# Kernel tuning notes

Hardware: AMD Instinct MI355X
Metric: run time of the kernel (lower is better)

Reference implementation:

```python
import jax, jax.numpy as jnp
import numpy as np

N = 100000
E = 800000
D_IN = 64
D_OUT = 64
SCALES = (4, 8)


def setup_inputs() -> dict:
    key = jax.random.key(0)
    ks = jax.random.split(key, 8)
    x = jax.random.normal(ks[0], (N, D_IN), dtype=jnp.float32)
    edge_index = jax.random.randint(ks[1], (2, E), 0, N, dtype=jnp.int64)
    s = 1.0 / np.sqrt(D_IN)
    W1 = jax.random.uniform(ks[2], (D_OUT, D_IN), minval=-s, maxval=s, dtype=jnp.float32)
    b1 = jax.random.uniform(ks[3], (D_OUT,), minval=-s, maxval=s, dtype=jnp.float32)
    W2 = jax.random.uniform(ks[4], (D_OUT, D_IN), minval=-s, maxval=s, dtype=jnp.float32)
    b2 = jax.random.uniform(ks[5], (D_OUT,), minval=-s, maxval=s, dtype=jnp.float32)
    sg = 1.0 / np.sqrt(D_OUT * len(SCALES))
    Wg = jax.random.uniform(ks[6], (D_OUT, D_OUT * len(SCALES)), minval=-sg, maxval=sg, dtype=jnp.float32)
    bg = jax.random.uniform(ks[7], (D_OUT,), minval=-sg, maxval=sg, dtype=jnp.float32)
    return {"x": x, "edge_index": edge_index, "W1": W1, "b1": b1,
            "W2": W2, "b2": b2, "Wg": Wg, "bg": bg}


def _gconv(x, src, tgt, W, b):
    # scatter-add neighbor features: agg[src] += x[tgt]
    agg = jax.ops.segment_sum(x[tgt], src, num_segments=N)  # [N, D_IN]
    counts = jax.ops.segment_sum(jnp.ones((src.shape[0], 1), x.dtype), src,
                                 num_segments=N) + 1e-6     # [N, 1]
    agg = agg / counts
    return agg @ W.T + b                                    # [N, D_OUT]


def reference(x, edge_index, W1, b1, W2, b2, Wg, bg):
    k_max = E // N  # = 8
    outs = []
    for scale, (W, b) in zip(SCALES, ((W1, b1), (W2, b2))):
        scale = min(scale, k_max)
        src = edge_index[0, :N * scale]
        tgt = edge_index[1, :N * scale]
        outs.append(_gconv(x, src, tgt, W, b))
    multi = jnp.concatenate(outs, axis=-1)                   # [N, 2*D_OUT]
    gate = jax.nn.sigmoid(multi @ Wg.T + bg)                 # [N, D_OUT]
    fused = gate * outs[0] + (1.0 - gate) * outs[1]
    return fused
```

## Files before the change

### kernel.cpp

```cpp
#include <hip/hip_runtime.h>
#include <hip/hip_bf16.h>

#define N_NODES 100000
#define E_TOTAL 800000
#define E1      400000
#define D       64
#define CAP     32

#define NPB        256
#define NB         ((N_NODES + NPB - 1) / NPB)
#define BSTRIDE    (NPB * CAP)
#define BCAP       3072
#define EPB        4096
#define NBKT_BLKS  ((E_TOTAL + EPB - 1) / EPB)

typedef short s16x8 __attribute__((ext_vector_type(8)));
typedef float f32x4 __attribute__((ext_vector_type(4)));
typedef unsigned u32x4 __attribute__((ext_vector_type(4)));

#define WS_CNT     0
#define WS_ENTRIES (N_NODES)
#define WS_W1B     (WS_ENTRIES + N_NODES * CAP)
#define WS_W2B     (WS_W1B + 2048)
#define WS_WGB     (WS_W2B + 2048)
#define WS_BIAS    (WS_WGB + 4096)
#define WS_CUR     (WS_BIAS + 192)
#define WS_XB      (WS_CUR + 400)
#define WS_NEED_BYTES ((size_t)(WS_XB + (size_t)N_NODES * D / 2) * 4)

#define R_X   (N_NODES * D / 8)
#define R_W   (R_X + 2048)
#define R_B   (R_W + 24)
#define CONV_BLOCKS ((R_B + 255) / 256)

__device__ __forceinline__ float ldv(const void* p, size_t idx, int fp32)
{
    return fp32 ? ((const float*)p)[idx]
                : __bfloat162float(((const __hip_bfloat16*)p)[idx]);
}

__device__ __forceinline__ void detect2(const int* ei, const unsigned short* xu,
                                        int* s2, int& e64, int& fp32)
{
    if (threadIdx.x == 0) { s2[0] = 0; s2[1] = 0; }
    __syncthreads();
    if (threadIdx.x < 16 && ei[2 * threadIdx.x + 1] != 0) atomicOr(&s2[0], 1);
    { unsigned u = xu[threadIdx.x]; if (((u >> 7) & 0xFF) >= 0x90) atomicOr(&s2[1], 1); }
    __syncthreads();
    e64 = (s2[0] == 0); fp32 = s2[1];
}

__global__ __launch_bounds__(256) void prep_kernel(
    const void* __restrict__ xv, const int* __restrict__ ei,
    const void* __restrict__ W1v, const void* __restrict__ b1v,
    const void* __restrict__ W2v, const void* __restrict__ b2v,
    const void* __restrict__ Wgv, const void* __restrict__ bgv,
    unsigned* __restrict__ ws, int use_xb)
{
    __shared__ int s2[2];
    __shared__ unsigned hist[NB];
    __shared__ unsigned bbase[NB];
    int e64, fp32;
    detect2(ei, (const unsigned short*)xv, s2, e64, fp32);

    if (blockIdx.x < NBKT_BLKS) {
        for (int j = threadIdx.x; j < NB; j += 256) hist[j] = 0;
        __syncthreads();

        const int e0 = blockIdx.x * EPB;
        int srcv[16], tgtv[16];
#pragma unroll
        for (int i = 0; i < 16; ++i) {
            const int e = e0 + i * 256 + threadIdx.x;
            srcv[i] = -1;
            if (e < E_TOTAL) {
                if (e64) {
                    srcv[i] = (int)((const uint2*)ei)[e].x;
                    tgtv[i] = (int)((const uint2*)ei)[E_TOTAL + e].x;
                } else {
                    srcv[i] = ei[e]; tgtv[i] = ei[E_TOTAL + e];
                }
            }
        }
        unsigned recv[16], br[16];
#pragma unroll
        for (int i = 0; i < 16; ++i) {
            const int e = e0 + i * 256 + threadIdx.x;
            br[i] = 0xFFFFFFFFu;
            if (srcv[i] >= 0) {
                const unsigned b = (unsigned)srcv[i] >> 8;
                const unsigned r = atomicAdd(&hist[b], 1u);
                recv[i] = (unsigned)tgtv[i]
                        | ((e < E1) ? (1u << 17) : 0u)
                        | (((unsigned)srcv[i] & (NPB - 1)) << 18);
                br[i] = (b << 16) | r;
            }
        }
        __syncthreads();
        for (int j = threadIdx.x; j < NB; j += 256) {
            const unsigned h = hist[j];
            bbase[j] = h ? atomicAdd(ws + WS_CUR + j, h) : 0u;
        }
        __syncthreads();
#pragma unroll
        for (int i = 0; i < 16; ++i) {
            if (br[i] != 0xFFFFFFFFu) {
                const unsigned b = br[i] >> 16, r = br[i] & 0xFFFFu;
                const unsigned pos = bbase[b] + r;
                if (pos < BCAP)
                    ws[WS_ENTRIES + (size_t)b * BSTRIDE + pos] = recv[i];
            }
        }
        return;
    }

    const int gid = (blockIdx.x - NBKT_BLKS) * 256 + threadIdx.x;
    __hip_bfloat16* Xb  = (__hip_bfloat16*)(ws + WS_XB);
    __hip_bfloat16* W1b = (__hip_bfloat16*)(ws + WS_W1B);
    __hip_bfloat16* W2b = (__hip_bfloat16*)(ws + WS_W2B);
    __hip_bfloat16* Wgb = (__hip_bfloat16*)(ws + WS_WGB);
    float* bias = (float*)(ws + WS_BIAS);

    if (gid < R_X) {
        if (use_xb && fp32) {
            const f32x4 v0 = ((const f32x4*)xv)[2 * gid];
            const f32x4 v1 = ((const f32x4*)xv)[2 * gid + 1];
            s16x8 o;
#pragma unroll
            for (int j = 0; j < 4; ++j) {
                o[j]     = (short)__bfloat16_as_ushort(__float2bfloat16(v0[j]));
                o[4 + j] = (short)__bfloat16_as_ushort(__float2bfloat16(v1[j]));
            }
            *(s16x8*)(Xb + (size_t)gid * 8) = o;
        }
    } else if (gid < R_W) {
        const int j = gid - R_X;
#pragma unroll
        for (int k = 0; k < 8; ++k) {
            const int i = j * 8 + k;
            if (i < 4096)       W1b[i]        = __float2bfloat16(ldv(W1v, i, fp32));
            else if (i < 8192)  W2b[i - 4096] = __float2bfloat16(ldv(W2v, i - 4096, fp32));
            else                Wgb[i - 8192] = __float2bfloat16(ldv(Wgv, i - 8192, fp32));
        }
    } else if (gid < R_B) {
        const int j = gid - R_W;
#pragma unroll
        for (int k = 0; k < 8; ++k) {
            const int i = j * 8 + k;
            if (i < 64)       bias[i] = ldv(b1v, i, fp32);
            else if (i < 128) bias[i] = ldv(b2v, i - 64, fp32);
            else              bias[i] = ldv(bgv, i - 128, fp32);
        }
    }
}

__global__ __launch_bounds__(256) void csr_kernel(unsigned* __restrict__ ws)
{
    __shared__ unsigned cnt_l[NPB];
    __shared__ __align__(16) unsigned ent[NPB * CAP];

    const int b  = blockIdx.x;
    const int n0 = b * NPB;
    const int nn = min(NPB, N_NODES - n0);

    cnt_l[threadIdx.x] = 0;
    __syncthreads();

    const unsigned C = min(ws[WS_CUR + b], (unsigned)BCAP);
    for (unsigned r = threadIdx.x; r < C; r += 256) {
        const unsigned rec = ws[WS_ENTRIES + (size_t)b * BSTRIDE + r];
        const unsigned sl  = rec >> 18;
        const unsigned p   = atomicAdd(&cnt_l[sl], 1u);
        if (p < CAP)
            ent[sl * CAP + p] = (rec & 0x1FFFFu) | ((rec & (1u << 17)) ? 0x80000000u : 0u);
    }
    __syncthreads();

    const int tot4 = (nn * CAP) / 4;
    u32x4* dst = (u32x4*)(ws + WS_ENTRIES + (size_t)n0 * CAP);
    const u32x4* srcp = (const u32x4*)ent;
    for (int j = threadIdx.x; j < tot4; j += 256) dst[j] = srcp[j];

    if (threadIdx.x < nn) ws[WS_CNT + n0 + threadIdx.x] = cnt_l[threadIdx.x];
}

__global__ __launch_bounds__(256) void fused_kernel(
    const unsigned* __restrict__ ws, const void* __restrict__ xv,
    void* __restrict__ outv, int use_xb)
{
    __shared__ __align__(16) __hip_bfloat16 sS[16][136];
    __shared__ __align__(16) __hip_bfloat16 sO[16][136];
    __shared__ int s2d[2];

    if (threadIdx.x == 0) s2d[0] = 0;
    __syncthreads();
    { unsigned u = ((const unsigned short*)xv)[threadIdx.x];
      if (((u >> 7) & 0xFF) >= 0x90) atomicOr(&s2d[0], 1); }
    __syncthreads();
    const int fp32 = s2d[0];

    const int w    = threadIdx.x >> 6;
    const int lane = threadIdx.x & 63;
    const int base = blockIdx.x * 16;

    const int direct_f32 = (fp32 && !use_xb);
    const char* xb = (use_xb && fp32) ? (const char*)(ws + WS_XB) : (const char*)xv;
    const float* xf = (const float*)xv;

    unsigned eraw[4], entv[4], degr[4]; int degc[4];
#pragma unroll
    for (int i = 0; i < 4; ++i) {
        const int n = base + w * 4 + i;
        degr[i] = ws[WS_CNT + n];
        eraw[i] = (lane < CAP) ? ws[WS_ENTRIES + (size_t)n * CAP + lane] : 0u;
    }
#pragma unroll
    for (int i = 0; i < 4; ++i) {
        degc[i] = (int)min(degr[i], (unsigned)CAP);
        entv[i] = (lane < degc[i]) ? eraw[i] : 0u;
    }

    const int half = lane >> 5;
    const int cc   = lane & 31;

    if (!direct_f32) {
        int c1[4];
#pragma unroll
        for (int i = 0; i < 4; ++i)
            c1[i] = (int)__popcll(__ballot(entv[i] & 0x80000000u));

        float s1x[4], s1y[4], s2x[4], s2y[4];
#pragma unroll
        for (int i = 0; i < 4; ++i) { s1x[i] = s1y[i] = s2x[i] = s2y[i] = 0.f; }

        int rmax = 0;
#pragma unroll
        for (int i = 0; i < 4; ++i) rmax = max(rmax, (degc[i] + 1) >> 1);

#pragma unroll 2
        for (int r = 0; r < rmax; ++r) {
#pragma unroll
            for (int i = 0; i < 4; ++i) {
                const int j = 2 * r + half;
                const unsigned en = __shfl(entv[i], j);
                if (j < degc[i]) {
                    const unsigned off = ((en & 0x7FFFFFFFu) << 7) + ((unsigned)cc << 2);
                    const unsigned u = *(const unsigned*)(xb + off);
                    const float fx = __uint_as_float(u << 16);
                    const float fy = __uint_as_float(u & 0xFFFF0000u);
                    const float fl = (en & 0x80000000u) ? 1.f : 0.f;
                    s2x[i] += fx; s2y[i] += fy;
                    s1x[i] = fmaf(fl, fx, s1x[i]); s1y[i] = fmaf(fl, fy, s1y[i]);
                }
            }
        }

#pragma unroll
        for (int i = 0; i < 4; ++i) {
            const int nl = w * 4 + i;
            float a = s1x[i], b = s1y[i], c = s2x[i], d = s2y[i];
            a += __shfl_xor(a, 32); b += __shfl_xor(b, 32);
            c += __shfl_xor(c, 32); d += __shfl_xor(d, 32);
            const float inv1 = 1.0f / ((float)c1[i] + 1e-6f);
            const float inv2 = 1.0f / ((float)degr[i] + 1e-6f);
            if (lane < 32) {
                const __hip_bfloat162 p1 = __float22bfloat162_rn({a * inv1, b * inv1});
                const __hip_bfloat162 p2 = __float22bfloat162_rn({c * inv2, d * inv2});
                *(__hip_bfloat162*)&sS[nl][2 * cc]      = p1;
                *(__hip_bfloat162*)&sS[nl][64 + 2 * cc] = p2;
            }
        }
    } else {
#pragma unroll
        for (int i = 0; i < 4; ++i) {
            const int nl = w * 4 + i;
            const int c1 = (int)__popcll(__ballot(entv[i] & 0x80000000u));
            float s1x = 0.f, s2x = 0.f;
            for (int j = 0; j < degc[i]; ++j) {
                const unsigned en = __builtin_amdgcn_readlane(entv[i], j);
                const float v = xf[(size_t)(en & 0x7FFFFFFFu) * D + lane];
                s2x += v;
                if (en & 0x80000000u) s1x += v;
            }
            const float inv1 = 1.0f / ((float)c1 + 1e-6f);
            const float inv2 = 1.0f / ((float)degr[i] + 1e-6f);
            sS[nl][lane]      = __float2bfloat16(s1x * inv1);
            sS[nl][64 + lane] = __float2bfloat16(s2x * inv2);
        }
    }
    __syncthreads();

    const int m = lane & 15;
    const int q = lane >> 4;
    const int nd = w * 16 + m;

    const s16x8* W1b = (const s16x8*)(ws + WS_W1B);
    const s16x8* W2b = (const s16x8*)(ws + WS_W2B);
    const s16x8* Wgb = (const s16x8*)(ws + WS_WGB);
    const float* bias = (const float*)(ws + WS_BIAS);

    const s16x8 a1c0 = *(const s16x8*)&sS[m][q * 8];
    const s16x8 a1c1 = *(const s16x8*)&sS[m][32 + q * 8];
    const s16x8 a2c0 = *(const s16x8*)&sS[m][64 + q * 8];
    const s16x8 a2c1 = *(const s16x8*)&sS[m][96 + q * 8];

    f32x4 z = {0.f, 0.f, 0.f, 0.f};
    z = __builtin_amdgcn_mfma_f32_16x16x32_bf16(a1c0, W1b[nd * 8 + q],     z, 0, 0, 0);
    z = __builtin_amdgcn_mfma_f32_16x16x32_bf16(a1c1, W1b[nd * 8 + 4 + q], z, 0, 0, 0);
    f32x4 y = {0.f, 0.f, 0.f, 0.f};
    y = __builtin_amdgcn_mfma_f32_16x16x32_bf16(a2c0, W2b[nd * 8 + q],     y, 0, 0, 0);
    y = __builtin_amdgcn_mfma_f32_16x16x32_bf16(a2c1, W2b[nd * 8 + 4 + q], y, 0, 0, 0);
    const float bb1 = bias[nd], bb2 = bias[64 + nd];
#pragma unroll
    for (int r = 0; r < 4; ++r) { z[r] += bb1; y[r] += bb2; }

#pragma unroll
    for (int r = 0; r < 4; ++r) {
        sO[q * 4 + r][nd]      = __float2bfloat16(z[r]);
        sO[q * 4 + r][64 + nd] = __float2bfloat16(y[r]);
    }
    __syncthreads();

    s16x8 ga[4];
#pragma unroll
    for (int c = 0; c < 4; ++c)
        ga[c] = *(const s16x8*)&sO[m][c * 32 + q * 8];

    f32x4 g4 = {0.f, 0.f, 0.f, 0.f};
#pragma unroll
    for (int c = 0; c < 4; ++c)
        g4 = __builtin_amdgcn_mfma_f32_16x16x32_bf16(ga[c], Wgb[nd * 16 + c * 4 + q], g4, 0, 0, 0);
    const float bbg = bias[128 + nd];

#pragma unroll
    for (int r = 0; r < 4; ++r) {
        const float g = 1.0f / (1.0f + __expf(-(g4[r] + bbg)));
        const float v = g * z[r] + (1.0f - g) * y[r];
        const size_t node = (size_t)(base + q * 4 + r);
        if (fp32) ((float*)outv)[node * 64 + nd] = v;
        else      ((__hip_bfloat16*)outv)[node * 64 + nd] = __float2bfloat16(v);
    }
}

extern "C" void kernel_launch(void* const* d_in, const int* in_sizes, int n_in,
                              void* d_out, int out_size, void* d_ws, size_t ws_size,
                              hipStream_t stream)
{
    const void* x  = d_in[0];
    const int*  ei = (const int*)d_in[1];
    unsigned* ws = (unsigned*)d_ws;

    const int use_xb = (ws_size >= WS_NEED_BYTES) ? 1 : 0;

    hipMemsetAsync(ws + WS_CUR, 0, NB * sizeof(unsigned), stream);
    prep_kernel<<<NBKT_BLKS + CONV_BLOCKS, 256, 0, stream>>>(
        x, ei, d_in[2], d_in[3], d_in[4], d_in[5], d_in[6], d_in[7], ws, use_xb);
    csr_kernel<<<NB, 256, 0, stream>>>(ws);
    fused_kernel<<<N_NODES / 16, 256, 0, stream>>>(ws, x, d_out, use_xb);
}
```

Before: 171.6 us.

## Halve CSR bucket size, move x-to-bf16 conversion into CSR kernel, unroll gather

Bucket width drops from 256 to 128 nodes, which doubles the number of CSR blocks and halves the per-block shared-memory footprint. The fp32-to-bf16 conversion of x moves out of the edge-bucketing kernel and into the CSR kernel as extra blocks, to balance work across the two launches. The gather loop becomes branch-free: masked lanes load from row 0 and are zeroed, the trip count is rounded up to a multiple of four, and unrolling goes from 2 to 4 to expose more loads in flight. The cost is extra wasted loads in the padded iterations, and a per-bucket capacity of 1536 that could overflow if the edge distribution is skewed.

Result: faster. 150.8 us (-12.1%).

```diff
diff --git a/kernel.cpp b/kernel.cpp
--- a/kernel.cpp
+++ b/kernel.cpp
@@ -7,10 +7,10 @@
 #define D       64
 #define CAP     32
 
-#define NPB        256
+#define NPB        128
 #define NB         ((N_NODES + NPB - 1) / NPB)
 #define BSTRIDE    (NPB * CAP)
-#define BCAP       3072
+#define BCAP       1536
 #define EPB        4096
 #define NBKT_BLKS  ((E_TOTAL + EPB - 1) / EPB)
 
@@ -25,13 +25,14 @@
 #define WS_WGB     (WS_W2B + 2048)
 #define WS_BIAS    (WS_WGB + 4096)
 #define WS_CUR     (WS_BIAS + 192)
-#define WS_XB      (WS_CUR + 400)
+#define WS_XB      (WS_CUR + 800)
 #define WS_NEED_BYTES ((size_t)(WS_XB + (size_t)N_NODES * D / 2) * 4)
 
-#define R_X   (N_NODES * D / 8)
-#define R_W   (R_X + 2048)
-#define R_B   (R_W + 24)
-#define CONV_BLOCKS ((R_B + 255) / 256)
+#define PREP_CONV_THREADS (2048 + 24)
+#define PREP_CONV_BLOCKS  ((PREP_CONV_THREADS + 255) / 256)
+
+#define R_X          (N_NODES * D / 8)
+#define XCONV_BLOCKS (R_X / 256)
 
 __device__ __forceinline__ float ldv(const void* p, size_t idx, int fp32)
 {
@@ -55,7 +56,7 @@
     const void* __restrict__ W1v, const void* __restrict__ b1v,
     const void* __restrict__ W2v, const void* __restrict__ b2v,
     const void* __restrict__ Wgv, const void* __restrict__ bgv,
-    unsigned* __restrict__ ws, int use_xb)
+    unsigned* __restrict__ ws)
 {
     __shared__ int s2[2];
     __shared__ unsigned hist[NB];
@@ -88,7 +89,7 @@
             const int e = e0 + i * 256 + threadIdx.x;
             br[i] = 0xFFFFFFFFu;
             if (srcv[i] >= 0) {
-                const unsigned b = (unsigned)srcv[i] >> 8;
+                const unsigned b = (unsigned)srcv[i] >> 7;
                 const unsigned r = atomicAdd(&hist[b], 1u);
                 recv[i] = (unsigned)tgtv[i]
                         | ((e < E1) ? (1u << 17) : 0u)
@@ -115,35 +116,21 @@
     }
 
     const int gid = (blockIdx.x - NBKT_BLKS) * 256 + threadIdx.x;
-    __hip_bfloat16* Xb  = (__hip_bfloat16*)(ws + WS_XB);
     __hip_bfloat16* W1b = (__hip_bfloat16*)(ws + WS_W1B);
     __hip_bfloat16* W2b = (__hip_bfloat16*)(ws + WS_W2B);
     __hip_bfloat16* Wgb = (__hip_bfloat16*)(ws + WS_WGB);
     float* bias = (float*)(ws + WS_BIAS);
 
-    if (gid < R_X) {
-        if (use_xb && fp32) {
-            const f32x4 v0 = ((const f32x4*)xv)[2 * gid];
-            const f32x4 v1 = ((const f32x4*)xv)[2 * gid + 1];
-            s16x8 o;
-#pragma unroll
-            for (int j = 0; j < 4; ++j) {
-                o[j]     = (short)__bfloat16_as_ushort(__float2bfloat16(v0[j]));
-                o[4 + j] = (short)__bfloat16_as_ushort(__float2bfloat16(v1[j]));
-            }
-            *(s16x8*)(Xb + (size_t)gid * 8) = o;
-        }
-    } else if (gid < R_W) {
-        const int j = gid - R_X;
+    if (gid < 2048) {
 #pragma unroll
         for (int k = 0; k < 8; ++k) {
-            const int i = j * 8 + k;
+            const int i = gid * 8 + k;
             if (i < 4096)       W1b[i]        = __float2bfloat16(ldv(W1v, i, fp32));
             else if (i < 8192)  W2b[i - 4096] = __float2bfloat16(ldv(W2v, i - 4096, fp32));
             else                Wgb[i - 8192] = __float2bfloat16(ldv(Wgv, i - 8192, fp32));
         }
-    } else if (gid < R_B) {
-        const int j = gid - R_W;
+    } else if (gid < 2072) {
+        const int j = gid - 2048;
 #pragma unroll
         for (int k = 0; k < 8; ++k) {
             const int i = j * 8 + k;
@@ -154,34 +141,60 @@
     }
 }
 
-__global__ __launch_bounds__(256) void csr_kernel(unsigned* __restrict__ ws)
+__global__ __launch_bounds__(256) void csr_kernel(
+    const void* __restrict__ xv, unsigned* __restrict__ ws, int use_xb)
 {
     __shared__ unsigned cnt_l[NPB];
     __shared__ __align__(16) unsigned ent[NPB * CAP];
-
-    const int b  = blockIdx.x;
-    const int n0 = b * NPB;
-    const int nn = min(NPB, N_NODES - n0);
-
-    cnt_l[threadIdx.x] = 0;
-    __syncthreads();
-
-    const unsigned C = min(ws[WS_CUR + b], (unsigned)BCAP);
-    for (unsigned r = threadIdx.x; r < C; r += 256) {
-        const unsigned rec = ws[WS_ENTRIES + (size_t)b * BSTRIDE + r];
-        const unsigned sl  = rec >> 18;
-        const unsigned p   = atomicAdd(&cnt_l[sl], 1u);
-        if (p < CAP)
-            ent[sl * CAP + p] = (rec & 0x1FFFFu) | ((rec & (1u << 17)) ? 0x80000000u : 0u);
-    }
-    __syncthreads();
-
-    const int tot4 = (nn * CAP) / 4;
-    u32x4* dst = (u32x4*)(ws + WS_ENTRIES + (size_t)n0 * CAP);
-    const u32x4* srcp = (const u32x4*)ent;
-    for (int j = threadIdx.x; j < tot4; j += 256) dst[j] = srcp[j];
-
-    if (threadIdx.x < nn) ws[WS_CNT + n0 + threadIdx.x] = cnt_l[threadIdx.x];
+    __shared__ int s2[1];
+
+    if (blockIdx.x < NB) {
+        const int b  = blockIdx.x;
+        const int n0 = b * NPB;
+        const int nn = min(NPB, N_NODES - n0);
+
+        if (threadIdx.x < NPB) cnt_l[threadIdx.x] = 0;
+        __syncthreads();
+
+        const unsigned C = min(ws[WS_CUR + b], (unsigned)BCAP);
+        for (unsigned r = threadIdx.x; r < C; r += 256) {
+            const unsigned rec = ws[WS_ENTRIES + (size_t)b * BSTRIDE + r];
+            const unsigned sl  = rec >> 18;
+            const unsigned p   = atomicAdd(&cnt_l[sl], 1u);
+            if (p < CAP)
+                ent[sl * CAP + p] = (rec & 0x1FFFFu) | ((rec & (1u << 17)) ? 0x80000000u : 0u);
+        }
+        __syncthreads();
+
+        const int tot4 = (nn * CAP) / 4;
+        u32x4* dst = (u32x4*)(ws + WS_ENTRIES + (size_t)n0 * CAP);
+        const u32x4* srcp = (const u32x4*)ent;
+        for (int j = threadIdx.x; j < tot4; j += 256) dst[j] = srcp[j];
+
+        if (threadIdx.x < nn) ws[WS_CNT + n0 + threadIdx.x] = cnt_l[threadIdx.x];
+        return;
+    }
+
+    if (threadIdx.x == 0) s2[0] = 0;
+    __syncthreads();
+    { unsigned u = ((const unsigned short*)xv)[threadIdx.x];
+      if (((u >> 7) & 0xFF) >= 0x90) atomicOr(&s2[0], 1); }
+    __syncthreads();
+    const int fp32 = s2[0];
+
+    const int gid = (blockIdx.x - NB) * 256 + threadIdx.x;
+    if (gid < R_X && use_xb && fp32) {
+        __hip_bfloat16* Xb = (__hip_bfloat16*)(ws + WS_XB);
+        const f32x4 v0 = ((const f32x4*)xv)[2 * gid];
+        const f32x4 v1 = ((const f32x4*)xv)[2 * gid + 1];
+        s16x8 o;
+#pragma unroll
+        for (int j = 0; j < 4; ++j) {
+            o[j]     = (short)__bfloat16_as_ushort(__float2bfloat16(v0[j]));
+            o[4 + j] = (short)__bfloat16_as_ushort(__float2bfloat16(v1[j]));
+        }
+        *(s16x8*)(Xb + (size_t)gid * 8) = o;
+    }
 }
 
 __global__ __launch_bounds__(256) void fused_kernel(
@@ -236,22 +249,23 @@
         int rmax = 0;
 #pragma unroll
         for (int i = 0; i < 4; ++i) rmax = max(rmax, (degc[i] + 1) >> 1);
-
-#pragma unroll 2
+        rmax = (rmax + 3) & ~3;
+
+#pragma unroll 4
         for (int r = 0; r < rmax; ++r) {
 #pragma unroll
             for (int i = 0; i < 4; ++i) {
                 const int j = 2 * r + half;
-                const unsigned en = __shfl(entv[i], j);
-                if (j < degc[i]) {
-                    const unsigned off = ((en & 0x7FFFFFFFu) << 7) + ((unsigned)cc << 2);
-                    const unsigned u = *(const unsigned*)(xb + off);
-                    const float fx = __uint_as_float(u << 16);
-                    const float fy = __uint_as_float(u & 0xFFFF0000u);
-                    const float fl = (en & 0x80000000u) ? 1.f : 0.f;
-                    s2x[i] += fx; s2y[i] += fy;
-                    s1x[i] = fmaf(fl, fx, s1x[i]); s1y[i] = fmaf(fl, fy, s1y[i]);
-                }
+                unsigned en = __shfl(entv[i], j);
+                en = (j < degc[i]) ? en : 0u;
+                unsigned u = *(const unsigned*)(xb + ((size_t)(en & 0x7FFFFFFFu) << 7)
+                                                   + ((unsigned)cc << 2));
+                u = (j < degc[i]) ? u : 0u;
+                const float fx = __uint_as_float(u << 16);
+                const float fy = __uint_as_float(u & 0xFFFF0000u);
+                const float fl = (en & 0x80000000u) ? 1.f : 0.f;
+                s2x[i] += fx; s2y[i] += fy;
+                s1x[i] = fmaf(fl, fx, s1x[i]); s1y[i] = fmaf(fl, fy, s1y[i]);
             }
         }
 
@@ -352,9 +366,9 @@
 
     const int use_xb = (ws_size >= WS_NEED_BYTES) ? 1 : 0;
 
-    hipMemsetAsync(ws + WS_CUR, 0, NB * sizeof(unsigned), stream);
-    prep_kernel<<<NBKT_BLKS + CONV_BLOCKS, 256, 0, stream>>>(
-        x, ei, d_in[2], d_in[3], d_in[4], d_in[5], d_in[6], d_in[7], ws, use_xb);
-    csr_kernel<<<NB, 256, 0, stream>>>(ws);
+    hipMemsetAsync(ws + WS_CUR, 0, 800 * sizeof(unsigned), stream);
+    prep_kernel<<<NBKT_BLKS + PREP_CONV_BLOCKS, 256, 0, stream>>>(
+        x, ei, d_in[2], d_in[3], d_in[4], d_in[5], d_in[6], d_in[7], ws);
+    csr_kernel<<<NB + XCONV_BLOCKS, 256, 0, stream>>>(x, ws, use_xb);
     fused_kernel<<<N_NODES / 16, 256, 0, stream>>>(ws, x, d_out, use_xb);
 }
```
